# Kernel tuning notes

Hardware: AMD Instinct MI355X
Metric: run time of the kernel (lower is better)

Reference implementation:

```python
import jax, jax.numpy as jnp
import numpy as np
import math

B, CIN, H, W = 8, 64, 128, 128
IC = 128           # inter_channel
CMIN = 32
FN = 3             # feature_num
PLANES = CMIN * 2  # BNL planes
GROUPS = 8
ORDER = 2
GAMMA = 1e-4
FEAT_SHAPES = [(64, 128, 128), (128, 64, 64), (256, 32, 32)]

_pm_cache = {}

def _pool_mat(n, s):
    # adaptive avg-pool matrix [s, n] (torch AdaptiveAvgPool2d bin rule)
    key = (n, s)
    if key not in _pm_cache:
        m = np.zeros((s, n), np.float32)
        for j in range(s):
            a = (j * n) // s
            b = -((-(j + 1) * n) // s)
            m[j, a:b] = 1.0 / (b - a)
        _pm_cache[key] = jnp.asarray(m)
    return _pm_cache[key]

def _pap(x):
    # pyramidAP: adaptive avg pool to 1,3,6,8 and flatten -> [b,c,110]
    b, c, hh, ww = x.shape
    outs = []
    for s in (1, 3, 6, 8):
        ph, pw = _pool_mat(hh, s), _pool_mat(ww, s)
        outs.append(jnp.einsum('ph,bchw,qw->bcpq', ph, x, pw).reshape(b, c, s * s))
    return jnp.concatenate(outs, axis=2)

def _c1x1(w, x):
    return jnp.einsum('oi,bihw->bohw', w, x)

def _pad1(x):
    # kernel_size=1, padding=1 conv == 1x1 conv then zero-pad spatially by 1
    return jnp.pad(x, ((0, 0), (0, 0), (1, 1), (1, 1)))

def _conv3(w, x):
    return jax.lax.conv_general_dilated(x, w, (1, 1), 'SAME',
                                        dimension_numbers=('NCHW', 'OIHW', 'NCHW'))

def _bnl(x_high, x_low, t_w, p_w, g_w, z_w, gn_w, gn_b):
    b, c, h, w = x_high.shape
    # per-group flattened 'single token' vectors of length (planes/G)*h*w
    t = _c1x1(t_w, x_high).reshape(b, GROUPS, -1)
    p = _c1x1(p_w, x_low).reshape(b, GROUPS, -1)
    g = _c1x1(g_w, x_low).reshape(b, GROUPS, -1)
    alphas = [math.sqrt((2 * GAMMA) ** k / math.factorial(k) * math.exp(-2 * GAMMA))
              for k in range(ORDER + 1)]
    t_tay = jnp.stack([t ** k * alphas[k] for k in range(ORDER + 1)], axis=2)  # [b,G,3,N]
    p_tay = jnp.stack([p ** k * alphas[k] for k in range(ORDER + 1)], axis=2)
    att = jnp.einsum('bgkn,bgn->bgk', p_tay, g)          # [b,G,3]
    x = jnp.einsum('bgk,bgkn->bgn', att, t_tay).reshape(b, PLANES, h, w)
    # grouped 1x1 conv z (groups=8)
    x = jnp.einsum('goi,bgihw->bgohw', z_w,
                   x.reshape(b, GROUPS, PLANES // GROUPS, h, w)).reshape(b, c, h, w)
    # GroupNorm(8, 64)
    xg = x.reshape(b, GROUPS, -1)
    mu = xg.mean(-1, keepdims=True)
    var = xg.var(-1, keepdims=True)
    xn = ((xg - mu) / jnp.sqrt(var + 1e-5)).reshape(b, c, h, w)
    xn = xn * gn_w[None, :, None, None] + gn_b[None, :, None, None]
    return xn + x_high

def setup_inputs() -> dict:
    key = jax.random.key(0)
    ks = iter(jax.random.split(key, 64))
    def rn(shape, scale=1.0):
        return jax.random.normal(next(ks), shape, jnp.float32) * scale
    inp = {'input_g': rn((B, CIN, H, W)), 'input_c': rn((B, CIN, H, W))}
    for i, (c, hh, ww) in enumerate(FEAT_SHAPES):
        inp[f'fg_{i}'] = rn((B, c, hh, ww))
        inp[f'fc_{i}'] = rn((B, c, hh, ww))
        for nm in ('k1', 'v1', 'k2', 'v2'):
            inp[f'{nm}_w_{i}'] = rn((IC, c), 0.05)
    inp['q1_w'] = rn((IC, CIN, 3, 3), 0.05)
    inp['q2_w'] = rn((IC, CIN, 3, 3), 0.05)
    inp['mask1_w'] = rn((CIN, IC + CIN), 0.05)
    inp['mask2_w'] = rn((CIN, IC + CIN), 0.05)
    inp['fuse1_w'] = rn((CIN, CIN * FN), 0.05)
    inp['fuse2_w'] = rn((CIN, CIN * FN), 0.05)
    inp['t_w'] = rn((PLANES, CIN), 0.05)
    inp['p_w'] = rn((PLANES, CIN), 0.05)
    inp['g_w'] = rn((PLANES, CIN), 0.05)
    inp['z_w'] = rn((GROUPS, CIN // GROUPS, PLANES // GROUPS), 0.05)
    inp['gn_w'] = jnp.ones((CIN,), jnp.float32)
    inp['gn_b'] = jnp.zeros((CIN,), jnp.float32)
    return inp

def reference(input_g, input_c, fg_0, fg_1, fg_2, fc_0, fc_1, fc_2,
              q1_w, q2_w,
              k1_w_0, v1_w_0, k2_w_0, v2_w_0,
              k1_w_1, v1_w_1, k2_w_1, v2_w_1,
              k1_w_2, v1_w_2, k2_w_2, v2_w_2,
              mask1_w, mask2_w, fuse1_w, fuse2_w,
              t_w, p_w, g_w, z_w, gn_w, gn_b):
    b, c, h, w = input_g.shape
    n = h * w
    x_q1 = _conv3(q1_w, input_g).reshape(b, IC, n)
    x_q2 = _conv3(q2_w, input_c).reshape(b, IC, n)
    fgs = [fg_0, fg_1, fg_2]
    fcs = [fc_0, fc_1, fc_2]
    k1s = [k1_w_0, k1_w_1, k1_w_2]
    v1s = [v1_w_0, v1_w_1, v1_w_2]
    k2s = [k2_w_0, k2_w_1, k2_w_2]
    v2s = [v2_w_0, v2_w_1, v2_w_2]
    grays, colors = [], []
    for i in range(FN):
        xk1 = _pap(_pad1(_c1x1(k1s[i], fcs[i])))   # [b,IC,110]
        xk2 = _pap(_pad1(_c1x1(k2s[i], fgs[i])))
        xv1 = _pap(_pad1(_c1x1(v1s[i], fcs[i])))
        xv2 = _pap(_pad1(_c1x1(v2s[i], fgs[i])))
        kq1 = jax.nn.softmax(jnp.clip(jnp.einsum('bcp,bcn->bpn', xk1, x_q1), -64, 64), axis=1)
        kq2 = jax.nn.softmax(jnp.clip(jnp.einsum('bcp,bcn->bpn', xk2, x_q2), -64, 64), axis=1)
        vkq1 = jnp.einsum('bcp,bpn->bcn', xv1, kq1).reshape(b, IC, h, w)
        vkq2 = jnp.einsum('bcp,bpn->bcn', xv2, kq2).reshape(b, IC, h, w)
        grays.append(_c1x1(mask1_w, jnp.concatenate([input_g, vkq1], 1)))
        colors.append(_c1x1(mask2_w, jnp.concatenate([input_c, vkq2], 1)))
    x_gray = jnp.tanh(_c1x1(fuse1_w, jnp.concatenate(grays, 1))) + input_g
    x_color = jnp.tanh(_c1x1(fuse2_w, jnp.concatenate(colors, 1))) + input_c
    return _bnl(x_gray, x_color, t_w, p_w, g_w, z_w, gn_w, gn_b) + input_g
```

## Files before the change

### kernel.cpp

```cpp
#include <hip/hip_runtime.h>
#include <math.h>

constexpr int    BB      = 8;
constexpr int    NN      = 16384;
constexpr size_t SZ_XQ_ST = (size_t)BB * 128 * NN;
constexpr size_t SZ_XF_ST = (size_t)BB * 64 * NN;

constexpr size_t OFF_XQ   = 0;
constexpr size_t OFF_XT   = 16777216;
constexpr size_t OFF_XF   = 33554432;
constexpr size_t OFF_POOL = OFF_XF + 2 * SZ_XF_ST;
constexpr size_t OFF_XK   = OFF_POOL + 788480;
constexpr size_t OFF_XV   = OFF_XK + 344064;
constexpr size_t OFF_MT   = OFF_XV + 688128;
constexpr size_t OFF_W    = OFF_MT + 393216;
constexpr size_t OFF_AT   = OFF_W + 73728;
constexpr size_t OFF_WT   = OFF_AT + 4096;
constexpr size_t OFF_ATTC = OFF_WT + 12288;
constexpr size_t OFF_MV   = OFF_ATTC + 192;
constexpr size_t OFF_PART = OFF_MV + 128;

#define A0SQ 0.9998000199986667f
#define A1SQ 1.9996000399973335e-4f
#define A2SQ 1.9996000399973334e-8f

typedef __attribute__((ext_vector_type(8))) short bf16x8;
typedef __attribute__((ext_vector_type(4))) float f32x4;

__device__ inline ushort f2bf(float f) {
    uint u = __float_as_uint(f);
    return (ushort)((u + 0x7fffu + ((u >> 16) & 1u)) >> 16);
}
__device__ inline float bf2f(ushort u) { return __uint_as_float((uint)u << 16); }

__global__ __launch_bounds__(256) void k_xt(const float* __restrict__ in0, const float* __restrict__ in1,
                                            ushort* __restrict__ xt0, ushort* __restrict__ xt1) {
    __shared__ float L[64 * 130];
    const int y = blockIdx.x, b = blockIdx.y, tid = threadIdx.x;
    const float* in = blockIdx.z ? in1 : in0;
    ushort* xt = blockIdx.z ? xt1 : xt0;
    const float* ib = in + (((size_t)b * 64) << 14) + (y << 7);
    for (int r = 0; r < 32; ++r) {
        int idx = tid + (r << 8); int ch = idx >> 7; int x = idx & 127;
        L[ch * 130 + x] = ib[((size_t)ch << 14) + x];
    }
    __syncthreads();
    const int x = tid >> 1, seg = tid & 1;
    ushort* ob = xt + ((size_t)(b * 128 + y) * 128 + x) * 64 + seg * 32;
    uint pk[16];
#pragma unroll
    for (int c = 0; c < 16; ++c) {
        uint lo = f2bf(L[(seg * 32 + 2 * c) * 130 + x]);
        uint hi = f2bf(L[(seg * 32 + 2 * c + 1) * 130 + x]);
        pk[c] = lo | (hi << 16);
    }
    uint4* o4 = (uint4*)ob;
#pragma unroll
    for (int c = 0; c < 4; ++c) o4[c] = make_uint4(pk[4 * c], pk[4 * c + 1], pk[4 * c + 2], pk[4 * c + 3]);
}

__global__ __launch_bounds__(256) void k_wt(const float* __restrict__ w1, const float* __restrict__ w2,
                                            ushort* __restrict__ wt1, ushort* __restrict__ wt2) {
    int id = blockIdx.x * 256 + threadIdx.x;
    if (id >= 147456) return;
    int cs = id / 73728; int rem = id - cs * 73728;
    int t = rem >> 13; int oc = (rem >> 6) & 127; int ic = rem & 63;
    const float* w = cs ? w2 : w1;
    (cs ? wt2 : wt1)[rem] = f2bf(w[((size_t)(oc * 64 + ic)) * 9 + t]);
}

__global__ __launch_bounds__(256) void k_convm(const ushort* __restrict__ Xt0, const ushort* __restrict__ Xt1,
                                               const ushort* __restrict__ Wt0, const ushort* __restrict__ Wt1,
                                               ushort* __restrict__ out_base) {
    __shared__ ushort smem[2 * 128 * 72];
    ushort* lds_w = smem;
    ushort* lds_x = smem + 128 * 72;
    const int tid = threadIdx.x;
    const int y = blockIdx.x, b = blockIdx.y;
    const ushort* Xt = blockIdx.z ? Xt1 : Xt0;
    const ushort* Wt = blockIdx.z ? Wt1 : Wt0;
    ushort* out = out_base + (size_t)blockIdx.z * 16777216;
    const int l = tid & 63;
    const int wv = __builtin_amdgcn_readfirstlane(tid >> 6);
    const int lr = l & 15;
    const int q = l >> 4;
    const int cr = tid >> 1;
    const int seg = tid & 1;

    f32x4 acc[2][8];
#pragma unroll
    for (int f = 0; f < 2; ++f)
#pragma unroll
        for (int g = 0; g < 8; ++g)
#pragma unroll
            for (int r = 0; r < 4; ++r) acc[f][g][r] = 0.f;

#pragma unroll 1
    for (int t = 0; t < 9; ++t) {
        const int dy = t / 3, dx = t - dy * 3;
        const int srow = y + dy - 1;
        {
            const uint4* s = (const uint4*)(Wt + ((size_t)(t * 128 + cr) * 64 + seg * 32));
            uint4* d = (uint4*)(lds_w + cr * 72 + seg * 32);
            d[0] = s[0]; d[1] = s[1]; d[2] = s[2]; d[3] = s[3];
        }
        {
            const int sx = cr + dx - 1;
            const bool v = (srow >= 0) & (srow < 128) & (sx >= 0) & (sx < 128);
            const uint4* s = (const uint4*)(Xt + (((size_t)(b * 128 + srow) * 128 + sx) * 64 + seg * 32));
            uint4 z = make_uint4(0, 0, 0, 0);
            uint4 r0 = v ? s[0] : z, r1 = v ? s[1] : z, r2 = v ? s[2] : z, r3 = v ? s[3] : z;
            uint4* d = (uint4*)(lds_x + cr * 72 + seg * 32);
            d[0] = r0; d[1] = r1; d[2] = r2; d[3] = r3;
        }
        __syncthreads();
#pragma unroll
        for (int h = 0; h < 2; ++h) {
            const int ko = h * 32 + q * 8;
            bf16x8 a0 = *(const bf16x8*)(lds_w + (wv * 32 + lr) * 72 + ko);
            bf16x8 a1 = *(const bf16x8*)(lds_w + (wv * 32 + 16 + lr) * 72 + ko);
#pragma unroll
            for (int g = 0; g < 8; ++g) {
                bf16x8 bb = *(const bf16x8*)(lds_x + (g * 16 + lr) * 72 + ko);
                acc[0][g] = __builtin_amdgcn_mfma_f32_16x16x32_bf16(a0, bb, acc[0][g], 0, 0, 0);
                acc[1][g] = __builtin_amdgcn_mfma_f32_16x16x32_bf16(a1, bb, acc[1][g], 0, 0, 0);
            }
        }
        __syncthreads();
    }
    uint* T = (uint*)smem;
#pragma unroll
    for (int f = 0; f < 2; ++f)
#pragma unroll
        for (int g = 0; g < 8; ++g) {
            uint lo = (uint)f2bf(acc[f][g][0]) | ((uint)f2bf(acc[f][g][1]) << 16);
            uint hi = (uint)f2bf(acc[f][g][2]) | ((uint)f2bf(acc[f][g][3]) << 16);
            int dw = (g * 16 + lr) * 68 + wv * 16 + f * 8 + q * 2;
            T[dw] = lo; T[dw + 1] = hi;
        }
    __syncthreads();
    const int x = tid >> 1, sg = tid & 1;
    ushort* ob = out + ((size_t)(b * 128 + y) * 128 + x) * 128 + sg * 64;
    const uint* src = &T[x * 68 + sg * 32];
#pragma unroll
    for (int j = 0; j < 8; ++j) {
        uint4 vv = *(const uint4*)(src + 4 * j);
        *(uint4*)(ob + j * 8) = vv;
    }
}

struct PoolPtrs { const float* src[6]; };

__global__ __launch_bounds__(256) void k_pool(PoolPtrs pp, float* __restrict__ ws) {
    extern __shared__ float P[];
    const int plane = blockIdx.x;
    const int tid = threadIdx.x;
    int tI, h; size_t toff; int base;
    if      (plane < 512)  { tI = 0; h = 128; toff = 0;      base = 0;    }
    else if (plane < 1536) { tI = 1; h = 64;  toff = 56320;  base = 512;  }
    else if (plane < 3584) { tI = 2; h = 32;  toff = 168960; base = 1536; }
    else if (plane < 4096) { tI = 3; h = 128; toff = 394240; base = 3584; }
    else if (plane < 5120) { tI = 4; h = 64;  toff = 450560; base = 4096; }
    else                   { tI = 5; h = 32;  toff = 563200; base = 5120; }
    const int local = plane - base;
    const float* img = pp.src[tI] + (size_t)local * h * h;
    const int stride = h + 1;
    const int hh = h * h;
    for (int f = tid; f < hh; f += 256) {
        int r = f / h; int cc = f - r * h;
        P[r * stride + cc] = img[f];
    }
    __syncthreads();
    if (tid < h) {
        float cur = 0.f; const int rb = tid * stride;
        for (int cc = 0; cc < h; ++cc) { cur += P[rb + cc]; P[rb + cc] = cur; }
    }
    __syncthreads();
    if (tid < h) {
        float cur = 0.f;
        for (int r = 0; r < h; ++r) { int a = r * stride + tid; cur += P[a]; P[a] = cur; }
    }
    __syncthreads();
    if (tid < 110) {
        int s, off2;
        if (tid == 0)      { s = 1; off2 = 0; }
        else if (tid < 10) { s = 3; off2 = 1; }
        else if (tid < 46) { s = 6; off2 = 10; }
        else               { s = 8; off2 = 46; }
        int r = tid - off2; int j = r / s; int q = r - j * s;
        const int n = h + 2;
        int ra = (j * n) / s,       rb2 = ((j + 1) * n + s - 1) / s;
        int ca = (q * n) / s,       cb2 = ((q + 1) * n + s - 1) / s;
        float area = (float)((rb2 - ra) * (cb2 - ca));
        int r0 = ra - 1; if (r0 < 0) r0 = 0;  int r1 = rb2 - 1; if (r1 > h) r1 = h;
        int c0 = ca - 1; if (c0 < 0) c0 = 0;  int c1 = cb2 - 1; if (c1 > h) c1 = h;
        float ssum = 0.f;
        if (r1 > r0 && c1 > c0) {
            int ri = r1 - 1, rj = r0 - 1, ci = c1 - 1, cj = c0 - 1;
            float f11 = P[ri * stride + ci];
            float f01 = (rj < 0) ? 0.f : P[rj * stride + ci];
            float f10 = (cj < 0) ? 0.f : P[ri * stride + cj];
            float f00 = (rj < 0 || cj < 0) ? 0.f : P[rj * stride + cj];
            ssum = f11 - f01 - f10 + f00;
        }
        ws[OFF_POOL + toff + (size_t)local * 110 + tid] = ssum / area;
    }
}

__global__ __launch_bounds__(256) void k_pkw(const float* __restrict__ f1, const float* __restrict__ f2,
                                             const float* __restrict__ m1, const float* __restrict__ m2,
                                             const float* __restrict__ tw, const float* __restrict__ pw,
                                             const float* __restrict__ gw, float* __restrict__ ws) {
    int id = blockIdx.x * 256 + threadIdx.x;
    if (id < 73728) {
        int c = id % 192; int t = id / 192; int o = t & 63; int t2 = t >> 6; int i = t2 % 3; int st = t2 / 3;
        const float* fu = st ? f2 : f1; const float* ma = st ? m2 : m1;
        float s = 0.f;
        for (int k = 0; k < 64; ++k) s = fmaf(fu[o * 192 + i * 64 + k], ma[k * 192 + c], s);
        ws[OFF_W + id] = s;
    } else if (id < 81920) {
        int x = id - 73728; int o = x & 63; int c = (x >> 6) & 63; int st = x >> 12;
        const float* fu = st ? f2 : f1; const float* ma = st ? m2 : m1;
        float s = 0.f;
        for (int k = 0; k < 192; ++k) s = fmaf(fu[o * 192 + k], ma[(k & 63) * 192 + c], s);
        ((ushort*)(ws + OFF_AT))[(size_t)st * 4096 + o * 64 + c] = f2bf(s);
    } else if (id < 94208) {
        int x = id - 81920; int c = x & 63; int o = (x >> 6) & 63; int f = x >> 12;
        const float* src = (f == 0) ? tw : ((f == 1) ? pw : gw);
        ((ushort*)(ws + OFF_WT))[(size_t)f * 4096 + o * 64 + c] = f2bf(src[o * 64 + c]);
    }
}

struct KvPtrs { const float* k1[3]; const float* k2[3]; const float* v1[3]; const float* v2[3]; };

__global__ __launch_bounds__(256) void k_xkxv(KvPtrs kp, float* __restrict__ ws) {
    int id = blockIdx.x * 256 + threadIdx.x;
    int isV = 0;
    if (id >= 688128) { isV = 1; id -= 688128; }
    int p = id % 112; int t1 = id / 112; int C = t1 & 127; int t2 = t1 >> 7;
    int b = t2 & 7; int t3 = t2 >> 3; int i = t3 % 3; int st = t3 / 3;
    const int ci = 64 << i;
    size_t poff = (size_t)st * 394240 + (i >= 1 ? 56320 : 0) + (i >= 2 ? 112640 : 0);
    const float* kw = isV ? (st ? kp.v2[i] : kp.v1[i]) : (st ? kp.k2[i] : kp.k1[i]);
    float s = 0.f;
    if (p < 110) {
        const float* pl = ws + OFF_POOL + poff + (size_t)b * ci * 110 + p;
        for (int ic = 0; ic < ci; ++ic) s = fmaf(kw[C * ci + ic], pl[(size_t)ic * 110], s);
    }
    if (isV) ws[OFF_XV + id] = s;
    else     ((ushort*)(ws + OFF_XK))[(size_t)t2 * 14336 + p * 128 + C] = f2bf(s);
}

__global__ __launch_bounds__(256) void k_mt(float* __restrict__ ws) {
    int id = blockIdx.x * 256 + threadIdx.x;
    int p = id & 127; int o = (id >> 7) & 63; int t2 = id >> 13;
    int sti = t2 >> 3;
    float s = 0.f;
    if (p < 110) {
        const float* Wrow = ws + OFF_W + ((size_t)sti * 64 + o) * 192 + 64;
        const float* xv = ws + OFF_XV + (size_t)t2 * 128 * 112 + p;
        for (int r = 0; r < 128; ++r) s = fmaf(Wrow[r], xv[(size_t)r * 112], s);
    }
    ((ushort*)(ws + OFF_MT))[id] = f2bf(s);
}

__global__ __launch_bounds__(256, 2) void k_attn4(float* __restrict__ ws) {
    __shared__ uint pbuf[128 * 68];
    const int tid = threadIdx.x;
    const int w = __builtin_amdgcn_readfirstlane(tid >> 6);
    const int l = tid & 63;
    const int lr = l & 15;
    const int g4 = l >> 4;
    const int n0 = blockIdx.x << 7;
    const int b = blockIdx.y;
    const int st = blockIdx.z;

    const ushort* xqb = (const ushort*)(ws + OFF_XQ);
    const ushort* xkb = (const ushort*)(ws + OFF_XK);
    const ushort* mtb = (const ushort*)(ws + OFF_MT);
    const ushort* atb = (const ushort*)(ws + OFF_AT) + (size_t)st * 4096;
    const ushort* xt  = (const ushort*)(ws + OFF_XT) + (size_t)st * 8388608 + ((size_t)b << 14) * 64;
    ushort* xfb       = (ushort*)(ws + OFF_XF) + (size_t)st * 8388608 + ((size_t)b << 14) * 64;

    {
        int row = w * 32 + (l >> 1);
        int dcol = 56 + ((l & 1) << 2);
#pragma unroll
        for (int j = 0; j < 4; ++j) pbuf[row * 68 + dcol + j] = 0;
    }
    const int ng0 = n0 + (2 * w + 0) * 16 + lr;
    const int ng1 = n0 + (2 * w + 1) * 16 + lr;
    const int row0 = w * 32 + lr;
    const int row1 = w * 32 + 16 + lr;

    bf16x8 bq[2][4];
    {
        const ushort* p0 = xqb + ((size_t)(st * 8 + b) * 16384 + ng0) * 128 + g4 * 8;
        const ushort* p1 = xqb + ((size_t)(st * 8 + b) * 16384 + ng1) * 128 + g4 * 8;
#pragma unroll
        for (int kk = 0; kk < 4; ++kk) { bq[0][kk] = *(const bf16x8*)(p0 + kk * 32); bq[1][kk] = *(const bf16x8*)(p1 + kk * 32); }
    }

    f32x4 pacc[4][2];
#pragma unroll
    for (int m = 0; m < 4; ++m)
#pragma unroll
        for (int nt = 0; nt < 2; ++nt)
#pragma unroll
            for (int r = 0; r < 4; ++r) pacc[m][nt][r] = 0.f;

#pragma unroll
    for (int kk = 0; kk < 2; ++kk) {
        bf16x8 bi0 = *(const bf16x8*)(xt + (size_t)ng0 * 64 + kk * 32 + g4 * 8);
        bf16x8 bi1 = *(const bf16x8*)(xt + (size_t)ng1 * 64 + kk * 32 + g4 * 8);
#pragma unroll
        for (int m = 0; m < 4; ++m) {
            bf16x8 a = *(const bf16x8*)(atb + (m * 16 + lr) * 64 + kk * 32 + g4 * 8);
            pacc[m][0] = __builtin_amdgcn_mfma_f32_16x16x32_bf16(a, bi0, pacc[m][0], 0, 0, 0);
            pacc[m][1] = __builtin_amdgcn_mfma_f32_16x16x32_bf16(a, bi1, pacc[m][1], 0, 0, 0);
        }
    }

#pragma unroll 1
    for (int i = 0; i < 3; ++i) {
        const ushort* xk = xkb + (size_t)((st * 3 + i) * 8 + b) * 14336 + (size_t)lr * 128 + g4 * 8;
        const ushort* mt_p = mtb + (size_t)((st * 3 + i) * 8 + b) * 8192 + (size_t)lr * 128 + g4 * 8;
        f32x4 sacc[7][2];
#pragma unroll
        for (int m = 0; m < 7; ++m)
#pragma unroll
            for (int nt = 0; nt < 2; ++nt)
#pragma unroll
                for (int r = 0; r < 4; ++r) sacc[m][nt][r] = 0.f;
        bf16x8 ac[7], an[7];
#pragma unroll
        for (int m = 0; m < 7; ++m) ac[m] = *(const bf16x8*)(xk + (size_t)(m * 16) * 128);
#pragma unroll
        for (int kk = 0; kk < 4; ++kk) {
            if (kk < 3) {
#pragma unroll
                for (int m = 0; m < 7; ++m) an[m] = *(const bf16x8*)(xk + (size_t)(m * 16) * 128 + (kk + 1) * 32);
            }
#pragma unroll
            for (int m = 0; m < 7; ++m) {
                sacc[m][0] = __builtin_amdgcn_mfma_f32_16x16x32_bf16(ac[m], bq[0][kk], sacc[m][0], 0, 0, 0);
                sacc[m][1] = __builtin_amdgcn_mfma_f32_16x16x32_bf16(ac[m], bq[1][kk], sacc[m][1], 0, 0, 0);
            }
            if (kk < 3) {
#pragma unroll
                for (int m = 0; m < 7; ++m) ac[m] = an[m];
            }
        }
        bf16x8 mc[4], mn[4];
#pragma unroll
        for (int m = 0; m < 4; ++m) mc[m] = *(const bf16x8*)(mt_p + (size_t)(m * 16) * 128);
#pragma unroll
        for (int nt = 0; nt < 2; ++nt) {
            float mx = -3.0e38f;
#pragma unroll
            for (int m = 0; m < 7; ++m)
#pragma unroll
                for (int r = 0; r < 4; ++r) {
                    int p = m * 16 + g4 * 4 + r;
                    float s = fminf(fmaxf(sacc[m][nt][r], -64.f), 64.f);
                    if (p >= 110) s = -3.0e38f;
                    sacc[m][nt][r] = s;
                    mx = fmaxf(mx, s);
                }
            mx = fmaxf(mx, __shfl_xor(mx, 16));
            mx = fmaxf(mx, __shfl_xor(mx, 32));
            float sum = 0.f;
#pragma unroll
            for (int m = 0; m < 7; ++m)
#pragma unroll
                for (int r = 0; r < 4; ++r) {
                    float e = __expf(sacc[m][nt][r] - mx);
                    sacc[m][nt][r] = e;
                    sum += e;
                }
            sum += __shfl_xor(sum, 16);
            sum += __shfl_xor(sum, 32);
            float inv = 1.f / sum;
            const int rowNT = (nt == 0) ? row0 : row1;
#pragma unroll
            for (int m = 0; m < 7; ++m) {
                uint lo = (uint)f2bf(sacc[m][nt][0] * inv) | ((uint)f2bf(sacc[m][nt][1] * inv) << 16);
                uint hi = (uint)f2bf(sacc[m][nt][2] * inv) | ((uint)f2bf(sacc[m][nt][3] * inv) << 16);
                int dw = rowNT * 68 + m * 8 + g4 * 2;
                pbuf[dw] = lo; pbuf[dw + 1] = hi;
            }
        }
#pragma unroll
        for (int kk = 0; kk < 4; ++kk) {
            if (kk < 3) {
#pragma unroll
                for (int m = 0; m < 4; ++m) mn[m] = *(const bf16x8*)(mt_p + (size_t)(m * 16) * 128 + (kk + 1) * 32);
            }
            bf16x8 pb0 = *(const bf16x8*)((const ushort*)pbuf + (size_t)row0 * 136 + kk * 32 + g4 * 8);
            bf16x8 pb1 = *(const bf16x8*)((const ushort*)pbuf + (size_t)row1 * 136 + kk * 32 + g4 * 8);
#pragma unroll
            for (int m = 0; m < 4; ++m) {
                pacc[m][0] = __builtin_amdgcn_mfma_f32_16x16x32_bf16(mc[m], pb0, pacc[m][0], 0, 0, 0);
                pacc[m][1] = __builtin_amdgcn_mfma_f32_16x16x32_bf16(mc[m], pb1, pacc[m][1], 0, 0, 0);
            }
            if (kk < 3) {
#pragma unroll
                for (int m = 0; m < 4; ++m) mc[m] = mn[m];
            }
        }
    }
#pragma unroll
    for (int nt = 0; nt < 2; ++nt) {
        const int ng = (nt == 0) ? ng0 : ng1;
#pragma unroll
        for (int m = 0; m < 4; ++m) {
            const ushort4 gi4 = *(const ushort4*)(xt + (size_t)ng * 64 + m * 16 + g4 * 4);
            uint pk[2];
#pragma unroll
            for (int h = 0; h < 2; ++h) {
                float v0 = pacc[m][nt][2 * h];
                float v1 = pacc[m][nt][2 * h + 1];
                float x0 = fminf(fmaxf(v0, -15.f), 15.f);
                float x1 = fminf(fmaxf(v1, -15.f), 15.f);
                float e0 = __expf(2.f * x0), e1 = __expf(2.f * x1);
                float t0 = __fdividef(e0 - 1.f, e0 + 1.f) + bf2f(h ? gi4.z : gi4.x);
                float t1 = __fdividef(e1 - 1.f, e1 + 1.f) + bf2f(h ? gi4.w : gi4.y);
                pk[h] = (uint)f2bf(t0) | ((uint)f2bf(t1) << 16);
            }
            *(uint2*)(xfb + (size_t)ng * 64 + m * 16 + g4 * 4) = make_uint2(pk[0], pk[1]);
        }
    }
}

__global__ __launch_bounds__(256) void k_tpg(float* __restrict__ ws) {
    const int tid = threadIdx.x;
    const int w = __builtin_amdgcn_readfirstlane(tid >> 6);
    const int l = tid & 63;
    const int lr = l & 15;
    const int g4 = l >> 4;
    const int nb = blockIdx.x; const int n0 = nb << 7; const int b = blockIdx.y;

    const ushort* xfg = (const ushort*)(ws + OFF_XF) + ((size_t)b << 14) * 64;
    const ushort* xfc = xfg + 8388608;
    const ushort* wtb = (const ushort*)(ws + OFF_WT);
    float* tf = ws + OFF_XQ + ((size_t)b << 14) * 64;

    float s[4][3];
#pragma unroll
    for (int m = 0; m < 4; ++m) { s[m][0] = 0.f; s[m][1] = 0.f; s[m][2] = 0.f; }

#pragma unroll 1
    for (int nt = 0; nt < 2; ++nt) {
        const int ng = n0 + (2 * w + nt) * 16 + lr;
        f32x4 at_[4], ap_[4], ag_[4];
#pragma unroll
        for (int m = 0; m < 4; ++m)
#pragma unroll
            for (int r = 0; r < 4; ++r) { at_[m][r] = 0.f; ap_[m][r] = 0.f; ag_[m][r] = 0.f; }
#pragma unroll
        for (int kk = 0; kk < 2; ++kk) {
            bf16x8 bg = *(const bf16x8*)(xfg + (size_t)ng * 64 + kk * 32 + g4 * 8);
            bf16x8 bc = *(const bf16x8*)(xfc + (size_t)ng * 64 + kk * 32 + g4 * 8);
#pragma unroll
            for (int m = 0; m < 4; ++m) {
                const int ao = (m * 16 + lr) * 64 + kk * 32 + g4 * 8;
                bf16x8 a_t = *(const bf16x8*)(wtb + ao);
                bf16x8 a_p = *(const bf16x8*)(wtb + 4096 + ao);
                bf16x8 a_g = *(const bf16x8*)(wtb + 8192 + ao);
                at_[m] = __builtin_amdgcn_mfma_f32_16x16x32_bf16(a_t, bg, at_[m], 0, 0, 0);
                ap_[m] = __builtin_amdgcn_mfma_f32_16x16x32_bf16(a_p, bc, ap_[m], 0, 0, 0);
                ag_[m] = __builtin_amdgcn_mfma_f32_16x16x32_bf16(a_g, bc, ag_[m], 0, 0, 0);
            }
        }
#pragma unroll
        for (int m = 0; m < 4; ++m)
#pragma unroll
            for (int r = 0; r < 4; ++r) {
                int o = m * 16 + g4 * 4 + r;
                tf[((size_t)o << 14) + ng] = at_[m][r];
                float pv = ap_[m][r], gv = ag_[m][r];
                s[m][0] += gv;
                s[m][1] = fmaf(pv, gv, s[m][1]);
                s[m][2] = fmaf(pv * pv, gv, s[m][2]);
            }
    }
#pragma unroll
    for (int off = 1; off < 32; off <<= 1)
#pragma unroll
        for (int m = 0; m < 4; ++m)
#pragma unroll
            for (int k = 0; k < 3; ++k) s[m][k] += __shfl_xor(s[m][k], off);
    if (l == 0 || l == 32) {
        const int h = g4 >> 1;
#pragma unroll
        for (int m = 0; m < 4; ++m)
#pragma unroll
            for (int k = 0; k < 3; ++k)
                ws[OFF_PART + (size_t)((b * 8 + 2 * m + h) * 3 + k) * 512 + nb * 4 + w] = s[m][k];
    }
}

__global__ __launch_bounds__(64) void k_attc(float* __restrict__ ws) {
    const int id = blockIdx.x;
    const int l = threadIdx.x;
    const float4* v = (const float4*)(ws + OFF_PART + (size_t)id * 512 + l * 8);
    float4 a = v[0], b2 = v[1];
    float s = a.x + a.y + a.z + a.w + b2.x + b2.y + b2.z + b2.w;
#pragma unroll
    for (int off = 1; off < 64; off <<= 1) s += __shfl_xor(s, off);
    if (l == 0) ws[OFF_ATTC + id] = s;
}

__global__ __launch_bounds__(256) void k_stats(float* __restrict__ ws, const float* __restrict__ zw) {
    __shared__ float r0[256], r1[256];
    const int g = blockIdx.x, b = blockIdx.y, tid = threadIdx.x;
    const float* tf = ws + OFF_XQ + ((size_t)(b * 64 + g * 8) << 14);
    const float* a = ws + OFF_ATTC + (size_t)(b * 8 + g) * 3;
    const float c0 = A0SQ * a[0], c1 = A1SQ * a[1], c2 = A2SQ * a[2];
    const float* z = zw + (size_t)g * 64;
    float sum = 0.f, ssq = 0.f;
    for (int n = tid; n < 16384; n += 256) {
        float y[8];
#pragma unroll
        for (int pl = 0; pl < 8; ++pl) { float tv = tf[((size_t)pl << 14) + n]; y[pl] = fmaf(fmaf(c2, tv, c1), tv, c0); }
#pragma unroll
        for (int o = 0; o < 8; ++o) {
            float xz = 0.f;
#pragma unroll
            for (int i2 = 0; i2 < 8; ++i2) xz = fmaf(z[o * 8 + i2], y[i2], xz);
            sum += xz; ssq = fmaf(xz, xz, ssq);
        }
    }
    r0[tid] = sum; r1[tid] = ssq;
    __syncthreads();
    for (int w = 128; w > 0; w >>= 1) {
        if (tid < w) { r0[tid] += r0[tid + w]; r1[tid] += r1[tid + w]; }
        __syncthreads();
    }
    if (tid == 0) {
        float mean = r0[0] * (1.f / 131072.f);
        float var = r1[0] * (1.f / 131072.f) - mean * mean;
        float* mv = ws + OFF_MV + (size_t)(b * 8 + g) * 2;
        mv[0] = mean; mv[1] = rsqrtf(var + 1e-5f);
    }
}

__global__ __launch_bounds__(256) void k_final(float* __restrict__ ws, const float* __restrict__ zw,
                                               const float* __restrict__ gnw, const float* __restrict__ gnb,
                                               const float* __restrict__ g_in, float* __restrict__ out) {
    int id = blockIdx.x * 256 + threadIdx.x;
    int n = id & 16383; int g = (id >> 14) & 7; int b = id >> 17;
    const float* a = ws + OFF_ATTC + (size_t)(b * 8 + g) * 3;
    const float c0 = A0SQ * a[0], c1 = A1SQ * a[1], c2 = A2SQ * a[2];
    const float* mv = ws + OFF_MV + (size_t)(b * 8 + g) * 2;
    const float mean = mv[0], istd = mv[1];
    const float* z = zw + (size_t)g * 64;
    const float* tf = ws + OFF_XQ + ((size_t)(b * 64 + g * 8) << 14) + n;
    float y[8];
#pragma unroll
    for (int pl = 0; pl < 8; ++pl) { float tv = tf[(size_t)pl << 14]; y[pl] = fmaf(fmaf(c2, tv, c1), tv, c0); }
    const ushort* xgb = (const ushort*)(ws + OFF_XF) + (((size_t)b << 14) + n) * 64 + g * 8;
    ushort4 u0 = *(const ushort4*)xgb;
    ushort4 u1 = *(const ushort4*)(xgb + 4);
    float xgv[8] = { bf2f(u0.x), bf2f(u0.y), bf2f(u0.z), bf2f(u0.w),
                     bf2f(u1.x), bf2f(u1.y), bf2f(u1.z), bf2f(u1.w) };
    const size_t cb = ((size_t)(b * 64 + g * 8) << 14) + n;
    const float* gi = g_in + cb;
    float* op = out + cb;
#pragma unroll
    for (int o = 0; o < 8; ++o) {
        float xz = 0.f;
#pragma unroll
        for (int i2 = 0; i2 < 8; ++i2) xz = fmaf(z[o * 8 + i2], y[i2], xz);
        int ch = g * 8 + o;
        float v = fmaf((xz - mean) * istd, gnw[ch], gnb[ch]) + xgv[o] + gi[(size_t)o << 14];
        op[(size_t)o << 14] = v;
    }
}

extern "C" void kernel_launch(void* const* d_in, const int* in_sizes, int n_in,
                              void* d_out, int out_size, void* d_ws, size_t ws_size,
                              hipStream_t stream) {
    const float* in_g = (const float*)d_in[0];
    const float* in_c = (const float*)d_in[1];
    float* ws = (float*)d_ws;
    float* out = (float*)d_out;

    ushort* xqb  = (ushort*)(ws + OFF_XQ);
    ushort* xt_g = (ushort*)(ws + OFF_XT);
    ushort* xt_c = xt_g + 8388608;
    ushort* wt_g = (ushort*)(ws + OFF_XF);
    ushort* wt_c = wt_g + 73728;

    k_xt<<<dim3(128, 8, 2), 256, 0, stream>>>(in_g, in_c, xt_g, xt_c);
    k_wt<<<576, 256, 0, stream>>>((const float*)d_in[20], (const float*)d_in[21], wt_g, wt_c);

    k_convm<<<dim3(128, 8, 2), 256, 0, stream>>>(xt_g, xt_c, wt_g, wt_c, xqb);

    PoolPtrs pp;
    pp.src[0] = (const float*)d_in[3];  pp.src[1] = (const float*)d_in[9];  pp.src[2] = (const float*)d_in[15];
    pp.src[3] = (const float*)d_in[2];  pp.src[4] = (const float*)d_in[8];  pp.src[5] = (const float*)d_in[14];
    k_pool<<<7168, 256, 128 * 129 * 4, stream>>>(pp, ws);

    k_pkw<<<368, 256, 0, stream>>>((const float*)d_in[24], (const float*)d_in[25],
                                   (const float*)d_in[22], (const float*)d_in[23],
                                   (const float*)d_in[26], (const float*)d_in[27],
                                   (const float*)d_in[28], ws);

    KvPtrs kp;
    kp.k1[0] = (const float*)d_in[4];  kp.k1[1] = (const float*)d_in[10]; kp.k1[2] = (const float*)d_in[16];
    kp.k2[0] = (const float*)d_in[6];  kp.k2[1] = (const float*)d_in[12]; kp.k2[2] = (const float*)d_in[18];
    kp.v1[0] = (const float*)d_in[5];  kp.v1[1] = (const float*)d_in[11]; kp.v1[2] = (const float*)d_in[17];
    kp.v2[0] = (const float*)d_in[7];  kp.v2[1] = (const float*)d_in[13]; kp.v2[2] = (const float*)d_in[19];
    k_xkxv<<<5376, 256, 0, stream>>>(kp, ws);

    k_mt<<<3072, 256, 0, stream>>>(ws);

    k_attn4<<<dim3(128, 8, 2), 256, 0, stream>>>(ws);

    k_tpg<<<dim3(128, 8), 256, 0, stream>>>(ws);
    k_attc<<<192, 64, 0, stream>>>(ws);

    k_stats<<<dim3(8, 8), 256, 0, stream>>>(ws, (const float*)d_in[29]);
    k_final<<<4096, 256, 0, stream>>>(ws, (const float*)d_in[29], (const float*)d_in[30],
                                      (const float*)d_in[31], in_g, out);
}
```

Baseline: 576.1 us.

## Stage conv input rows once, split GroupNorm stats, keep fp32 residual

The 3x3 conv kernel now loads the three padded input rows into LDS once and reuses them for all nine taps. This removes the per-tap reload and barrier pairs, and weight fragments are read straight from global memory. GroupNorm statistics are split across 8 chunks per group with a small reduction kernel, so the old 64-block reduction gains more parallelism. The attention epilogue now adds the residual from the fp32 inputs instead of the bf16 transposed copy, and writes an fp32 x_gray buffer for the final kernel. That improves accuracy but costs extra traffic from the strided fp32 reads and writes.

```diff
diff --git a/kernel.cpp b/kernel.cpp
--- a/kernel.cpp
+++ b/kernel.cpp
@@ -9,6 +9,7 @@
 constexpr size_t OFF_XQ   = 0;
 constexpr size_t OFF_XT   = 16777216;
 constexpr size_t OFF_XF   = 33554432;
+constexpr size_t OFF_XG   = OFF_XF + 8388608;
 constexpr size_t OFF_POOL = OFF_XF + 2 * SZ_XF_ST;
 constexpr size_t OFF_XK   = OFF_POOL + 788480;
 constexpr size_t OFF_XV   = OFF_XK + 344064;
@@ -19,6 +20,7 @@
 constexpr size_t OFF_ATTC = OFF_WT + 12288;
 constexpr size_t OFF_MV   = OFF_ATTC + 192;
 constexpr size_t OFF_PART = OFF_MV + 128;
+constexpr size_t OFF_PART2= OFF_PART + 98304;
 
 #define A0SQ 0.9998000199986667f
 #define A1SQ 1.9996000399973335e-4f
@@ -69,12 +71,10 @@
     (cs ? wt2 : wt1)[rem] = f2bf(w[((size_t)(oc * 64 + ic)) * 9 + t]);
 }
 
-__global__ __launch_bounds__(256) void k_convm(const ushort* __restrict__ Xt0, const ushort* __restrict__ Xt1,
-                                               const ushort* __restrict__ Wt0, const ushort* __restrict__ Wt1,
-                                               ushort* __restrict__ out_base) {
-    __shared__ ushort smem[2 * 128 * 72];
-    ushort* lds_w = smem;
-    ushort* lds_x = smem + 128 * 72;
+__global__ __launch_bounds__(256, 2) void k_convm2(const ushort* __restrict__ Xt0, const ushort* __restrict__ Xt1,
+                                                   const ushort* __restrict__ Wt0, const ushort* __restrict__ Wt1,
+                                                   ushort* __restrict__ out_base) {
+    __shared__ ushort smem[3 * 130 * 72];
     const int tid = threadIdx.x;
     const int y = blockIdx.x, b = blockIdx.y;
     const ushort* Xt = blockIdx.z ? Xt1 : Xt0;
@@ -84,8 +84,18 @@
     const int wv = __builtin_amdgcn_readfirstlane(tid >> 6);
     const int lr = l & 15;
     const int q = l >> 4;
-    const int cr = tid >> 1;
-    const int seg = tid & 1;
+
+    for (int slot = tid; slot < 390; slot += 256) {
+        int dy = slot / 130, xx = slot - dy * 130;
+        int row = y + dy - 1, sx = xx - 1;
+        bool v = (row >= 0) & (row < 128) & (sx >= 0) & (sx < 128);
+        const uint4* s = (const uint4*)(Xt + (((size_t)(b * 128 + row) * 128 + sx) * 64));
+        uint4* d = (uint4*)(smem + (size_t)slot * 72);
+        uint4 z = make_uint4(0, 0, 0, 0);
+#pragma unroll
+        for (int j = 0; j < 8; ++j) d[j] = v ? s[j] : z;
+    }
+    __syncthreads();
 
     f32x4 acc[2][8];
 #pragma unroll
@@ -95,39 +105,23 @@
 #pragma unroll
             for (int r = 0; r < 4; ++r) acc[f][g][r] = 0.f;
 
-#pragma unroll 1
+#pragma unroll
     for (int t = 0; t < 9; ++t) {
         const int dy = t / 3, dx = t - dy * 3;
-        const int srow = y + dy - 1;
-        {
-            const uint4* s = (const uint4*)(Wt + ((size_t)(t * 128 + cr) * 64 + seg * 32));
-            uint4* d = (uint4*)(lds_w + cr * 72 + seg * 32);
-            d[0] = s[0]; d[1] = s[1]; d[2] = s[2]; d[3] = s[3];
-        }
-        {
-            const int sx = cr + dx - 1;
-            const bool v = (srow >= 0) & (srow < 128) & (sx >= 0) & (sx < 128);
-            const uint4* s = (const uint4*)(Xt + (((size_t)(b * 128 + srow) * 128 + sx) * 64 + seg * 32));
-            uint4 z = make_uint4(0, 0, 0, 0);
-            uint4 r0 = v ? s[0] : z, r1 = v ? s[1] : z, r2 = v ? s[2] : z, r3 = v ? s[3] : z;
-            uint4* d = (uint4*)(lds_x + cr * 72 + seg * 32);
-            d[0] = r0; d[1] = r1; d[2] = r2; d[3] = r3;
-        }
-        __syncthreads();
 #pragma unroll
         for (int h = 0; h < 2; ++h) {
             const int ko = h * 32 + q * 8;
-            bf16x8 a0 = *(const bf16x8*)(lds_w + (wv * 32 + lr) * 72 + ko);
-            bf16x8 a1 = *(const bf16x8*)(lds_w + (wv * 32 + 16 + lr) * 72 + ko);
+            bf16x8 a0 = *(const bf16x8*)(Wt + ((size_t)(t * 128 + wv * 32 + lr) * 64 + ko));
+            bf16x8 a1 = *(const bf16x8*)(Wt + ((size_t)(t * 128 + wv * 32 + 16 + lr) * 64 + ko));
 #pragma unroll
             for (int g = 0; g < 8; ++g) {
-                bf16x8 bb = *(const bf16x8*)(lds_x + (g * 16 + lr) * 72 + ko);
+                bf16x8 bb = *(const bf16x8*)(smem + (size_t)(dy * 130 + g * 16 + lr + dx) * 72 + ko);
                 acc[0][g] = __builtin_amdgcn_mfma_f32_16x16x32_bf16(a0, bb, acc[0][g], 0, 0, 0);
                 acc[1][g] = __builtin_amdgcn_mfma_f32_16x16x32_bf16(a1, bb, acc[1][g], 0, 0, 0);
             }
         }
-        __syncthreads();
-    }
+    }
+    __syncthreads();
     uint* T = (uint*)smem;
 #pragma unroll
     for (int f = 0; f < 2; ++f)
@@ -264,7 +258,9 @@
     ((ushort*)(ws + OFF_MT))[id] = f2bf(s);
 }
 
-__global__ __launch_bounds__(256, 2) void k_attn4(float* __restrict__ ws) {
+__global__ __launch_bounds__(256, 2) void k_attn4(float* __restrict__ ws,
+                                                  const float* __restrict__ g_in,
+                                                  const float* __restrict__ c_in) {
     __shared__ uint pbuf[128 * 68];
     const int tid = threadIdx.x;
     const int w = __builtin_amdgcn_readfirstlane(tid >> 6);
@@ -409,25 +405,28 @@
             }
         }
     }
+    const float* ginf = (st ? c_in : g_in) + (((size_t)b * 64) << 14);
+    float* xgf = ws + OFF_XG + ((size_t)b << 14) * 64;
 #pragma unroll
     for (int nt = 0; nt < 2; ++nt) {
         const int ng = (nt == 0) ? ng0 : ng1;
 #pragma unroll
         for (int m = 0; m < 4; ++m) {
-            const ushort4 gi4 = *(const ushort4*)(xt + (size_t)ng * 64 + m * 16 + g4 * 4);
-            uint pk[2];
-#pragma unroll
-            for (int h = 0; h < 2; ++h) {
-                float v0 = pacc[m][nt][2 * h];
-                float v1 = pacc[m][nt][2 * h + 1];
-                float x0 = fminf(fmaxf(v0, -15.f), 15.f);
-                float x1 = fminf(fmaxf(v1, -15.f), 15.f);
-                float e0 = __expf(2.f * x0), e1 = __expf(2.f * x1);
-                float t0 = __fdividef(e0 - 1.f, e0 + 1.f) + bf2f(h ? gi4.z : gi4.x);
-                float t1 = __fdividef(e1 - 1.f, e1 + 1.f) + bf2f(h ? gi4.w : gi4.y);
-                pk[h] = (uint)f2bf(t0) | ((uint)f2bf(t1) << 16);
-            }
-            *(uint2*)(xfb + (size_t)ng * 64 + m * 16 + g4 * 4) = make_uint2(pk[0], pk[1]);
+            float o4[4];
+#pragma unroll
+            for (int r = 0; r < 4; ++r) {
+                int o = m * 16 + g4 * 4 + r;
+                float v = pacc[m][nt][r];
+                float xx = fminf(fmaxf(v, -15.f), 15.f);
+                float e = __expf(2.f * xx);
+                float th = __fdividef(e - 1.f, e + 1.f);
+                o4[r] = th + ginf[((size_t)o << 14) + ng];
+            }
+            uint lo = (uint)f2bf(o4[0]) | ((uint)f2bf(o4[1]) << 16);
+            uint hi = (uint)f2bf(o4[2]) | ((uint)f2bf(o4[3]) << 16);
+            *(uint2*)(xfb + (size_t)ng * 64 + m * 16 + g4 * 4) = make_uint2(lo, hi);
+            if (st == 0)
+                *(float4*)(xgf + (size_t)ng * 64 + m * 16 + g4 * 4) = make_float4(o4[0], o4[1], o4[2], o4[3]);
         }
     }
 }
@@ -511,15 +510,15 @@
     if (l == 0) ws[OFF_ATTC + id] = s;
 }
 
-__global__ __launch_bounds__(256) void k_stats(float* __restrict__ ws, const float* __restrict__ zw) {
+__global__ __launch_bounds__(256) void k_stats2(float* __restrict__ ws, const float* __restrict__ zw) {
     __shared__ float r0[256], r1[256];
-    const int g = blockIdx.x, b = blockIdx.y, tid = threadIdx.x;
+    const int nc = blockIdx.x, g = blockIdx.y, b = blockIdx.z, tid = threadIdx.x;
     const float* tf = ws + OFF_XQ + ((size_t)(b * 64 + g * 8) << 14);
     const float* a = ws + OFF_ATTC + (size_t)(b * 8 + g) * 3;
     const float c0 = A0SQ * a[0], c1 = A1SQ * a[1], c2 = A2SQ * a[2];
     const float* z = zw + (size_t)g * 64;
     float sum = 0.f, ssq = 0.f;
-    for (int n = tid; n < 16384; n += 256) {
+    for (int n = nc * 2048 + tid; n < (nc + 1) * 2048; n += 256) {
         float y[8];
 #pragma unroll
         for (int pl = 0; pl < 8; ++pl) { float tv = tf[((size_t)pl << 14) + n]; y[pl] = fmaf(fmaf(c2, tv, c1), tv, c0); }
@@ -538,11 +537,21 @@
         __syncthreads();
     }
     if (tid == 0) {
-        float mean = r0[0] * (1.f / 131072.f);
-        float var = r1[0] * (1.f / 131072.f) - mean * mean;
-        float* mv = ws + OFF_MV + (size_t)(b * 8 + g) * 2;
-        mv[0] = mean; mv[1] = rsqrtf(var + 1e-5f);
-    }
+        float* p2 = ws + OFF_PART2 + (size_t)((b * 8 + g) * 8 + nc) * 2;
+        p2[0] = r0[0]; p2[1] = r1[0];
+    }
+}
+
+__global__ __launch_bounds__(64) void k_mv(float* __restrict__ ws) {
+    const int t = threadIdx.x;
+    float sum = 0.f, ssq = 0.f;
+    const float* p2 = ws + OFF_PART2 + (size_t)t * 16;
+#pragma unroll
+    for (int nc = 0; nc < 8; ++nc) { sum += p2[nc * 2]; ssq += p2[nc * 2 + 1]; }
+    float mean = sum * (1.f / 131072.f);
+    float var = ssq * (1.f / 131072.f) - mean * mean;
+    float* mv = ws + OFF_MV + (size_t)t * 2;
+    mv[0] = mean; mv[1] = rsqrtf(var + 1e-5f);
 }
 
 __global__ __launch_bounds__(256) void k_final(float* __restrict__ ws, const float* __restrict__ zw,
@@ -559,11 +568,10 @@
     float y[8];
 #pragma unroll
     for (int pl = 0; pl < 8; ++pl) { float tv = tf[(size_t)pl << 14]; y[pl] = fmaf(fmaf(c2, tv, c1), tv, c0); }
-    const ushort* xgb = (const ushort*)(ws + OFF_XF) + (((size_t)b << 14) + n) * 64 + g * 8;
-    ushort4 u0 = *(const ushort4*)xgb;
-    ushort4 u1 = *(const ushort4*)(xgb + 4);
-    float xgv[8] = { bf2f(u0.x), bf2f(u0.y), bf2f(u0.z), bf2f(u0.w),
-                     bf2f(u1.x), bf2f(u1.y), bf2f(u1.z), bf2f(u1.w) };
+    const float* xgf = ws + OFF_XG + (((size_t)b << 14) + n) * 64 + g * 8;
+    float4 x0 = *(const float4*)xgf;
+    float4 x1 = *(const float4*)(xgf + 4);
+    float xgv[8] = { x0.x, x0.y, x0.z, x0.w, x1.x, x1.y, x1.z, x1.w };
     const size_t cb = ((size_t)(b * 64 + g * 8) << 14) + n;
     const float* gi = g_in + cb;
     float* op = out + cb;
@@ -595,7 +603,7 @@
     k_xt<<<dim3(128, 8, 2), 256, 0, stream>>>(in_g, in_c, xt_g, xt_c);
     k_wt<<<576, 256, 0, stream>>>((const float*)d_in[20], (const float*)d_in[21], wt_g, wt_c);
 
-    k_convm<<<dim3(128, 8, 2), 256, 0, stream>>>(xt_g, xt_c, wt_g, wt_c, xqb);
+    k_convm2<<<dim3(128, 8, 2), 256, 0, stream>>>(xt_g, xt_c, wt_g, wt_c, xqb);
 
     PoolPtrs pp;
     pp.src[0] = (const float*)d_in[3];  pp.src[1] = (const float*)d_in[9];  pp.src[2] = (const float*)d_in[15];
@@ -616,12 +624,13 @@
 
     k_mt<<<3072, 256, 0, stream>>>(ws);
 
-    k_attn4<<<dim3(128, 8, 2), 256, 0, stream>>>(ws);
+    k_attn4<<<dim3(128, 8, 2), 256, 0, stream>>>(ws, in_g, in_c);
 
     k_tpg<<<dim3(128, 8), 256, 0, stream>>>(ws);
     k_attc<<<192, 64, 0, stream>>>(ws);
 
-    k_stats<<<dim3(8, 8), 256, 0, stream>>>(ws, (const float*)d_in[29]);
+    k_stats2<<<dim3(8, 8, 8), 256, 0, stream>>>(ws, (const float*)d_in[29]);
+    k_mv<<<1, 64, 0, stream>>>(ws);
     k_final<<<4096, 256, 0, stream>>>(ws, (const float*)d_in[29], (const float*)d_in[30],
                                       (const float*)d_in[31], in_g, out);
 }
```

Result: no change. 583.4 us (+1.3%).
